# Performance work log

Hardware: AMD Instinct MI355X
Metric: run time of the kernel (lower is better)

## Reference

```python
import jax, jax.numpy as jnp
import numpy as np

B, N, E0, F_IN, H, EMB, VEC, DPI = 1024, 256, 2048, 6, 32, 32, 26, 512


def setup_inputs() -> dict:
    key = jax.random.key(0)
    ks = jax.random.split(key, 16)
    # fixed urban scene graph, shared by every batch element, with self-loops
    src0 = jax.random.randint(ks[0], (E0,), 0, N, dtype=jnp.int32)
    dst0 = jax.random.randint(ks[1], (E0,), 0, N, dtype=jnp.int32)
    loops = jnp.arange(N, dtype=jnp.int32)
    src = jnp.concatenate([src0, loops])
    dst = jnp.concatenate([dst0, loops])

    s = 0.05
    return {
        "graph_feats": jax.random.normal(ks[2], (B, N, F_IN), jnp.float32),
        "vector": jax.random.normal(ks[3], (B, VEC), jnp.float32),
        "src": src,
        "dst": dst,
        "W1": jax.random.normal(ks[4], (F_IN, H), jnp.float32) * s,
        "b1": jnp.zeros((H,), jnp.float32),
        "W2": jax.random.normal(ks[5], (H, H), jnp.float32) * s,
        "b2": jnp.zeros((H,), jnp.float32),
        "W3": jax.random.normal(ks[6], (H, H), jnp.float32) * s,
        "b3": jnp.zeros((H,), jnp.float32),
        "W_emb": jax.random.normal(ks[7], (H, EMB), jnp.float32) * s,
        "b_emb": jnp.zeros((EMB,), jnp.float32),
        "W_pi": jax.random.normal(ks[8], (VEC + EMB, DPI), jnp.float32) * s,
        "b_pi": jnp.zeros((DPI,), jnp.float32),
        "W_vf": jax.random.normal(ks[9], (VEC + EMB, DPI), jnp.float32) * s,
        "b_vf": jnp.zeros((DPI,), jnp.float32),
    }


def _edge_norm(src, dst, n_nodes):
    # DGL GraphConv norm='both': out_deg(src)^-1/2 * in_deg(dst)^-1/2
    ones = jnp.ones(src.shape[0], jnp.float32)
    deg_out = jax.ops.segment_sum(ones, src, num_segments=n_nodes)
    deg_in = jax.ops.segment_sum(ones, dst, num_segments=n_nodes)
    inv_o = jnp.where(deg_out > 0, deg_out ** -0.5, 0.0)
    inv_i = jnp.where(deg_in > 0, deg_in ** -0.5, 0.0)
    return inv_o[src] * inv_i[dst]  # [E]


def _gconv(h, src, dst, norm, W, b):
    # h: [B, N, F]; symmetric-normalized aggregation then linear (DGL GraphConv)
    msg = h[:, src, :] * norm[None, :, None]          # [B, E, F]
    agg = jnp.zeros_like(h).at[:, dst, :].add(msg)     # [B, N, F]
    return agg @ W + b


def reference(graph_feats, vector, src, dst, W1, b1, W2, b2, W3, b3,
              W_emb, b_emb, W_pi, b_pi, W_vf, b_vf):
    n_nodes = graph_feats.shape[1]
    norm = _edge_norm(src, dst, n_nodes)
    h = jax.nn.relu(_gconv(graph_feats, src, dst, norm, W1, b1))
    h = jax.nn.relu(_gconv(h, src, dst, norm, W2, b2))
    h = jax.nn.relu(_gconv(h, src, dst, norm, W3, b3))  # three_layers=True
    hg = jnp.mean(h, axis=1)                 # dgl.mean_nodes -> [B, H]
    emb = hg @ W_emb + b_emb                 # [B, EMB]
    comb = jnp.concatenate([vector[:, :26], emb], axis=1)  # [B, 58]
    pi = jax.nn.relu(comb @ W_pi + b_pi)
    vf = jax.nn.relu(comb @ W_vf + b_vf)
    return pi, vf
```

## Files before the change

### kernel.cpp

```cpp
#include <hip/hip_runtime.h>
#include <hip/hip_fp16.h>

#define B_    1024
#define N_    256
#define E_    2304
#define EPT_  9
#define FIN_  6
#define VEC_  26
#define HSTR_ 40

typedef _Float16 half8 __attribute__((ext_vector_type(8)));
typedef float    f32x4 __attribute__((ext_vector_type(4)));

__global__ __launch_bounds__(256) void fused_kernel(
    const float* __restrict__ gf,
    const float* __restrict__ vec,
    const int* __restrict__ src, const int* __restrict__ dst,
    const float* __restrict__ W1, const float* __restrict__ b1,
    const float* __restrict__ W2, const float* __restrict__ b2,
    const float* __restrict__ W3, const float* __restrict__ b3,
    const float* __restrict__ We, const float* __restrict__ be,
    const float* __restrict__ Wpi, const float* __restrict__ bpi,
    const float* __restrict__ Wvf, const float* __restrict__ bvf,
    float2* __restrict__ out)
{
    __shared__ __align__(16) __half hbuf[N_ * HSTR_];
    __shared__ unsigned int packedE[E_];
    __shared__ float part[8 * 33];
    __shared__ float hgl[32];
    __shared__ float comb[VEC_ + 32];
    __shared__ int   wsum[4];

    const int t = threadIdx.x;
    const int b = blockIdx.x;
    const int lane = t & 63, wv = t >> 6;

    int*   deg_o  = (int*)hbuf;
    int*   deg_i  = (int*)hbuf + 256;
    int*   scanA  = (int*)hbuf + 512;
    int*   cursor = (int*)hbuf + 768;
    int*   perm   = (int*)hbuf + 1024;
    float* inv_o  = (float*)hbuf + 1280;
    float* inv_i  = (float*)hbuf + 1536;
    int*   bcnt   = (int*)hbuf + 1792;
    int*   boff   = (int*)hbuf + 1856;

    deg_o[t] = 0; deg_i[t] = 0;
    if (t < 64) bcnt[t] = 0;
    __syncthreads();

    int sB[EPT_], dB[EPT_];
#pragma unroll
    for (int i = 0; i < EPT_; ++i) { int e = t + 256 * i; sB[i] = src[e]; dB[i] = dst[e]; }
#pragma unroll
    for (int i = 0; i < EPT_; ++i) { atomicAdd(&deg_o[sB[i]], 1); atomicAdd(&deg_i[dB[i]], 1); }
    __syncthreads();

    const int dI = deg_i[t];
    {
        int dO = deg_o[t];
        inv_o[t] = dO > 0 ? rsqrtf((float)dO) : 0.f;
        inv_i[t] = dI > 0 ? rsqrtf((float)dI) : 0.f;
    }
    int x = dI;
#pragma unroll
    for (int d = 1; d < 64; d <<= 1) {
        int y = __shfl_up(x, d, 64);
        if (lane >= d) x += y;
    }
    if (lane == 63) wsum[wv] = x;
    const int bucket = dI > 63 ? 63 : dI;
    atomicAdd(&bcnt[bucket], 1);
    __syncthreads();

    {
        int prefix = 0;
#pragma unroll
        for (int w = 0; w < 3; ++w) if (w < wv) prefix += wsum[w];
        int incl = x + prefix;
        scanA[t]  = incl;
        cursor[t] = incl - dI;
    }
    if (t < 64) {
        int c = bcnt[t], xx = c;
#pragma unroll
        for (int d = 1; d < 64; d <<= 1) {
            int y = __shfl_up(xx, d, 64);
            if (lane >= d) xx += y;
        }
        boff[t] = xx - c;
    }
    __syncthreads();

    { int pos = atomicAdd(&boff[bucket], 1); perm[pos] = t; }
#pragma unroll
    for (int i = 0; i < EPT_; ++i) {
        int s = sB[i], dd = dB[i];
        int pos = atomicAdd(&cursor[dd], 1);
        float nrm = inv_o[s] * inv_i[dd];
        unsigned short h = __half_as_ushort(__float2half(nrm));
        packedE[pos] = ((unsigned int)s << 16) | (unsigned int)h;
    }
    __syncthreads();

    const int node = perm[t];
    const int end  = scanA[node];
    const int beg  = end - deg_i[node];
    __syncthreads();

    {
        const float* g = gf + (size_t)b * (N_ * FIN_);
        for (int i = t; i < N_ * 8; i += 256) {
            int n = i >> 3, k = i & 7;
            hbuf[n * HSTR_ + k] = __float2half((k < FIN_) ? g[n * FIN_ + k] : 0.f);
        }
    }
    __syncthreads();

    const __half2 z2 = __float2half2_rn(0.f);

    {
        __half2 a2[4] = {z2, z2, z2, z2};
        for (int e = beg; e < end; ++e) {
            unsigned int u = packedE[e];
            __half2 w2 = __half2half2(__ushort_as_half((unsigned short)(u & 0xffffu)));
            union { float4 f4; __half2 h2[4]; } r;
            r.f4 = *(const float4*)&hbuf[(u >> 16) * HSTR_];
#pragma unroll
            for (int q = 0; q < 4; ++q) a2[q] = __hfma2(w2, r.h2[q], a2[q]);
        }
        float a[FIN_], o[32];
#pragma unroll
        for (int k = 0; k < FIN_; ++k)
            a[k] = (k & 1) ? __high2float(a2[k >> 1]) : __low2float(a2[k >> 1]);
#pragma unroll
        for (int j = 0; j < 32; ++j) o[j] = b1[j];
#pragma unroll
        for (int k = 0; k < FIN_; ++k) {
            float ak = a[k];
            const float* wr = &W1[k * 32];
#pragma unroll
            for (int j = 0; j < 32; ++j) o[j] += ak * wr[j];
        }
        __syncthreads();
        union { float4 f4; __half2 h2[4]; } w;
        float4* row = (float4*)&hbuf[node * HSTR_];
#pragma unroll
        for (int q = 0; q < 4; ++q) {
#pragma unroll
            for (int r = 0; r < 4; ++r)
                w.h2[r] = __floats2half2_rn(fmaxf(o[8*q + 2*r], 0.f), fmaxf(o[8*q + 2*r + 1], 0.f));
            row[q] = w.f4;
        }
    }
    __syncthreads();

    const int m16  = lane & 15;
    const int q4   = lane >> 4;
    const int slab = wv * 64;

    for (int L = 0; L < 2; ++L) {
        const float* Wl = (L == 0) ? W2 : W3;
        const float* Bl = (L == 0) ? b2 : b3;

        half8 bfrag[2];
        float bias_c[2];
#pragma unroll
        for (int h = 0; h < 2; ++h) {
            int col = m16 + 16 * h;
#pragma unroll
            for (int j = 0; j < 8; ++j)
                bfrag[h][j] = (_Float16)Wl[(q4 * 8 + j) * 32 + col];
            bias_c[h] = Bl[col];
        }

        __half2 acc2[16];
#pragma unroll
        for (int j = 0; j < 16; ++j) acc2[j] = z2;
        for (int e = beg; e < end; ++e) {
            unsigned int u = packedE[e];
            __half2 w2 = __half2half2(__ushort_as_half((unsigned short)(u & 0xffffu)));
            const float4* hr = (const float4*)&hbuf[(u >> 16) * HSTR_];
            union { float4 f4; __half2 h2[4]; } r0, r1, r2, r3;
            r0.f4 = hr[0]; r1.f4 = hr[1]; r2.f4 = hr[2]; r3.f4 = hr[3];
#pragma unroll
            for (int q = 0; q < 4; ++q) {
                acc2[q]      = __hfma2(w2, r0.h2[q], acc2[q]);
                acc2[4 + q]  = __hfma2(w2, r1.h2[q], acc2[4 + q]);
                acc2[8 + q]  = __hfma2(w2, r2.h2[q], acc2[8 + q]);
                acc2[12 + q] = __hfma2(w2, r3.h2[q], acc2[12 + q]);
            }
        }
        __syncthreads();
        {
            union { float4 f4; __half2 h2[4]; } w;
            float4* row = (float4*)&hbuf[node * HSTR_];
#pragma unroll
            for (int q = 0; q < 4; ++q) {
#pragma unroll
                for (int r = 0; r < 4; ++r) w.h2[r] = acc2[4 * q + r];
                row[q] = w.f4;
            }
        }
        __syncthreads();

        half8 afrag[4];
#pragma unroll
        for (int g = 0; g < 4; ++g) {
            union { float4 f4; half8 h8; } u;
            u.f4 = *(const float4*)&hbuf[(slab + g * 16 + m16) * HSTR_ + q4 * 8];
            afrag[g] = u.h8;
        }
        f32x4 D[4][2];
#pragma unroll
        for (int g = 0; g < 4; ++g) {
#pragma unroll
            for (int h = 0; h < 2; ++h) {
                f32x4 c = {bias_c[h], bias_c[h], bias_c[h], bias_c[h]};
                D[g][h] = __builtin_amdgcn_mfma_f32_16x16x32_f16(afrag[g], bfrag[h], c, 0, 0, 0);
            }
        }
#pragma unroll
        for (int g = 0; g < 4; ++g) {
#pragma unroll
            for (int h = 0; h < 2; ++h) {
#pragma unroll
                for (int r = 0; r < 4; ++r) {
                    float v = fmaxf(D[g][h][r], 0.f);
                    hbuf[(slab + g * 16 + q4 * 4 + r) * HSTR_ + h * 16 + m16] = __float2half(v);
                }
            }
        }
        __syncthreads();
    }

    {
        int j = t & 31, g8 = t >> 5;
        float s = 0.f;
        for (int i = 0; i < 32; ++i)
            s += __half2float(hbuf[(g8 * 32 + i) * HSTR_ + j]);
        part[g8 * 33 + j] = s;
    }
    __syncthreads();
    if (t < 32) {
        float sum = 0.f;
#pragma unroll
        for (int g8 = 0; g8 < 8; ++g8) sum += part[g8 * 33 + t];
        hgl[t] = sum * (1.0f / 256.0f);
    }
    __syncthreads();

    if (t < 32) {
        float v = be[t];
#pragma unroll
        for (int j = 0; j < 32; ++j) v += hgl[j] * We[j * 32 + t];
        comb[VEC_ + t] = v;
    }
    if (t < VEC_) comb[t] = vec[b * VEC_ + t];
    __syncthreads();

    {
        float p0 = bpi[2 * t], p1 = bpi[2 * t + 1];
        float v0 = bvf[2 * t], v1 = bvf[2 * t + 1];
        const float2* Wp = (const float2*)Wpi;
        const float2* Wv = (const float2*)Wvf;
        for (int k = 0; k < VEC_ + 32; ++k) {
            float c = comb[k];
            float2 a = Wp[k * 256 + t];
            p0 += c * a.x; p1 += c * a.y;
            float2 d = Wv[k * 256 + t];
            v0 += c * d.x; v1 += c * d.y;
        }
        out[b * 256 + t]          = make_float2(fmaxf(p0, 0.f), fmaxf(p1, 0.f));
        out[262144 + b * 256 + t] = make_float2(fmaxf(v0, 0.f), fmaxf(v1, 0.f));
    }
}

extern "C" void kernel_launch(void* const* d_in, const int* in_sizes, int n_in,
                              void* d_out, int out_size, void* d_ws, size_t ws_size,
                              hipStream_t stream)
{
    fused_kernel<<<B_, 256, 0, stream>>>(
        (const float*)d_in[0], (const float*)d_in[1],
        (const int*)d_in[2], (const int*)d_in[3],
        (const float*)d_in[4], (const float*)d_in[5],
        (const float*)d_in[6], (const float*)d_in[7],
        (const float*)d_in[8], (const float*)d_in[9],
        (const float*)d_in[10], (const float*)d_in[11],
        (const float*)d_in[12], (const float*)d_in[13],
        (const float*)d_in[14], (const float*)d_in[15],
        (float2*)d_out);
}
```

Measured before the change: 119.0 us.

## Process two batch elements per block to amortize graph preprocessing

Each block now runs 512 threads and handles two batch elements. The degree counting, normalization, CSR sort and edge packing are done once by the first 256 threads and shared by both halves, which have separate hbuf slabs. In the final MLP each half computes one head (pi or vf) for both batch elements, so every weight load is reused across two samples. The cost is more shared memory per block (two 20KB hbufs) and idle threads during preprocessing, which may lower occupancy.

```diff
diff --git a/kernel.cpp b/kernel.cpp
--- a/kernel.cpp
+++ b/kernel.cpp
@@ -8,11 +8,12 @@
 #define FIN_  6
 #define VEC_  26
 #define HSTR_ 40
+#define BPB_  2
 
 typedef _Float16 half8 __attribute__((ext_vector_type(8)));
 typedef float    f32x4 __attribute__((ext_vector_type(4)));
 
-__global__ __launch_bounds__(256) void fused_kernel(
+__global__ __launch_bounds__(512) void fused_kernel(
     const float* __restrict__ gf,
     const float* __restrict__ vec,
     const int* __restrict__ src, const int* __restrict__ dst,
@@ -24,56 +25,65 @@
     const float* __restrict__ Wvf, const float* __restrict__ bvf,
     float2* __restrict__ out)
 {
-    __shared__ __align__(16) __half hbuf[N_ * HSTR_];
+    __shared__ __align__(16) __half hbuf[BPB_][N_ * HSTR_];
     __shared__ unsigned int packedE[E_];
-    __shared__ float part[8 * 33];
-    __shared__ float hgl[32];
-    __shared__ float comb[VEC_ + 32];
+    __shared__ float part[BPB_][8 * 33];
+    __shared__ float hgl[BPB_][32];
+    __shared__ float combS[BPB_][64];
     __shared__ int   wsum[4];
 
-    const int t = threadIdx.x;
-    const int b = blockIdx.x;
+    const int t  = threadIdx.x;
+    const int u  = t & 255;
+    const int bh = t >> 8;
+    const int b0 = blockIdx.x * BPB_;
     const int lane = t & 63, wv = t >> 6;
 
-    int*   deg_o  = (int*)hbuf;
-    int*   deg_i  = (int*)hbuf + 256;
-    int*   scanA  = (int*)hbuf + 512;
-    int*   cursor = (int*)hbuf + 768;
-    int*   perm   = (int*)hbuf + 1024;
-    float* inv_o  = (float*)hbuf + 1280;
-    float* inv_i  = (float*)hbuf + 1536;
-    int*   bcnt   = (int*)hbuf + 1792;
-    int*   boff   = (int*)hbuf + 1856;
-
-    deg_o[t] = 0; deg_i[t] = 0;
-    if (t < 64) bcnt[t] = 0;
+    int*   deg_o  = (int*)&hbuf[0][0];
+    int*   deg_i  = (int*)&hbuf[0][0] + 256;
+    int*   scanA  = (int*)&hbuf[0][0] + 512;
+    int*   cursor = (int*)&hbuf[0][0] + 768;
+    int*   perm   = (int*)&hbuf[0][0] + 1024;
+    float* inv_o  = (float*)&hbuf[0][0] + 1280;
+    float* inv_i  = (float*)&hbuf[0][0] + 1536;
+    int*   bcnt   = (int*)&hbuf[0][0] + 1792;
+    int*   boff   = (int*)&hbuf[0][0] + 1856;
+
+    if (t < 256) {
+        deg_o[t] = 0; deg_i[t] = 0;
+        if (t < 64) bcnt[t] = 0;
+    }
     __syncthreads();
 
     int sB[EPT_], dB[EPT_];
-#pragma unroll
-    for (int i = 0; i < EPT_; ++i) { int e = t + 256 * i; sB[i] = src[e]; dB[i] = dst[e]; }
-#pragma unroll
-    for (int i = 0; i < EPT_; ++i) { atomicAdd(&deg_o[sB[i]], 1); atomicAdd(&deg_i[dB[i]], 1); }
-    __syncthreads();
-
-    const int dI = deg_i[t];
-    {
-        int dO = deg_o[t];
-        inv_o[t] = dO > 0 ? rsqrtf((float)dO) : 0.f;
-        inv_i[t] = dI > 0 ? rsqrtf((float)dI) : 0.f;
-    }
-    int x = dI;
-#pragma unroll
-    for (int d = 1; d < 64; d <<= 1) {
-        int y = __shfl_up(x, d, 64);
-        if (lane >= d) x += y;
-    }
-    if (lane == 63) wsum[wv] = x;
-    const int bucket = dI > 63 ? 63 : dI;
-    atomicAdd(&bcnt[bucket], 1);
-    __syncthreads();
-
-    {
+    if (t < 256) {
+#pragma unroll
+        for (int i = 0; i < EPT_; ++i) { int e = t + 256 * i; sB[i] = src[e]; dB[i] = dst[e]; }
+#pragma unroll
+        for (int i = 0; i < EPT_; ++i) { atomicAdd(&deg_o[sB[i]], 1); atomicAdd(&deg_i[dB[i]], 1); }
+    }
+    __syncthreads();
+
+    int x = 0, dI = 0, bucket = 0;
+    if (t < 256) {
+        dI = deg_i[t];
+        {
+            int dO = deg_o[t];
+            inv_o[t] = dO > 0 ? rsqrtf((float)dO) : 0.f;
+            inv_i[t] = dI > 0 ? rsqrtf((float)dI) : 0.f;
+        }
+        x = dI;
+#pragma unroll
+        for (int d = 1; d < 64; d <<= 1) {
+            int y = __shfl_up(x, d, 64);
+            if (lane >= d) x += y;
+        }
+        if (lane == 63) wsum[wv] = x;
+        bucket = dI > 63 ? 63 : dI;
+        atomicAdd(&bcnt[bucket], 1);
+    }
+    __syncthreads();
+
+    if (t < 256) {
         int prefix = 0;
 #pragma unroll
         for (int w = 0; w < 3; ++w) if (w < wv) prefix += wsum[w];
@@ -92,27 +102,29 @@
     }
     __syncthreads();
 
-    { int pos = atomicAdd(&boff[bucket], 1); perm[pos] = t; }
-#pragma unroll
-    for (int i = 0; i < EPT_; ++i) {
-        int s = sB[i], dd = dB[i];
-        int pos = atomicAdd(&cursor[dd], 1);
-        float nrm = inv_o[s] * inv_i[dd];
-        unsigned short h = __half_as_ushort(__float2half(nrm));
-        packedE[pos] = ((unsigned int)s << 16) | (unsigned int)h;
-    }
-    __syncthreads();
-
-    const int node = perm[t];
+    if (t < 256) {
+        { int pos = atomicAdd(&boff[bucket], 1); perm[pos] = t; }
+#pragma unroll
+        for (int i = 0; i < EPT_; ++i) {
+            int s = sB[i], dd = dB[i];
+            int pos = atomicAdd(&cursor[dd], 1);
+            float nrm = inv_o[s] * inv_i[dd];
+            unsigned short hh = __half_as_ushort(__float2half(nrm));
+            packedE[pos] = ((unsigned int)s << 16) | (unsigned int)hh;
+        }
+    }
+    __syncthreads();
+
+    const int node = perm[u];
     const int end  = scanA[node];
     const int beg  = end - deg_i[node];
     __syncthreads();
 
     {
-        const float* g = gf + (size_t)b * (N_ * FIN_);
-        for (int i = t; i < N_ * 8; i += 256) {
+        const float* g = gf + (size_t)(b0 + bh) * (N_ * FIN_);
+        for (int i = u; i < N_ * 8; i += 256) {
             int n = i >> 3, k = i & 7;
-            hbuf[n * HSTR_ + k] = __float2half((k < FIN_) ? g[n * FIN_ + k] : 0.f);
+            hbuf[bh][n * HSTR_ + k] = __float2half((k < FIN_) ? g[n * FIN_ + k] : 0.f);
         }
     }
     __syncthreads();
@@ -122,29 +134,27 @@
     {
         __half2 a2[4] = {z2, z2, z2, z2};
         for (int e = beg; e < end; ++e) {
-            unsigned int u = packedE[e];
-            __half2 w2 = __half2half2(__ushort_as_half((unsigned short)(u & 0xffffu)));
+            unsigned int uu = packedE[e];
+            __half2 w2 = __half2half2(__ushort_as_half((unsigned short)(uu & 0xffffu)));
+            int ro = (uu >> 16) * HSTR_;
             union { float4 f4; __half2 h2[4]; } r;
-            r.f4 = *(const float4*)&hbuf[(u >> 16) * HSTR_];
+            r.f4 = *(const float4*)&hbuf[bh][ro];
 #pragma unroll
             for (int q = 0; q < 4; ++q) a2[q] = __hfma2(w2, r.h2[q], a2[q]);
         }
-        float a[FIN_], o[32];
-#pragma unroll
-        for (int k = 0; k < FIN_; ++k)
-            a[k] = (k & 1) ? __high2float(a2[k >> 1]) : __low2float(a2[k >> 1]);
+        float o[32];
 #pragma unroll
         for (int j = 0; j < 32; ++j) o[j] = b1[j];
 #pragma unroll
         for (int k = 0; k < FIN_; ++k) {
-            float ak = a[k];
+            float ak = (k & 1) ? __high2float(a2[k >> 1]) : __low2float(a2[k >> 1]);
             const float* wr = &W1[k * 32];
 #pragma unroll
             for (int j = 0; j < 32; ++j) o[j] += ak * wr[j];
         }
         __syncthreads();
         union { float4 f4; __half2 h2[4]; } w;
-        float4* row = (float4*)&hbuf[node * HSTR_];
+        float4* row = (float4*)&hbuf[bh][node * HSTR_];
 #pragma unroll
         for (int q = 0; q < 4; ++q) {
 #pragma unroll
@@ -157,7 +167,8 @@
 
     const int m16  = lane & 15;
     const int q4   = lane >> 4;
-    const int slab = wv * 64;
+    const int slab = (wv & 3) * 64;
+    const int wb   = wv >> 2;
 
     for (int L = 0; L < 2; ++L) {
         const float* Wl = (L == 0) ? W2 : W3;
@@ -166,21 +177,22 @@
         half8 bfrag[2];
         float bias_c[2];
 #pragma unroll
-        for (int h = 0; h < 2; ++h) {
-            int col = m16 + 16 * h;
+        for (int cb = 0; cb < 2; ++cb) {
+            int col = m16 + 16 * cb;
 #pragma unroll
             for (int j = 0; j < 8; ++j)
-                bfrag[h][j] = (_Float16)Wl[(q4 * 8 + j) * 32 + col];
-            bias_c[h] = Bl[col];
+                bfrag[cb][j] = (_Float16)Wl[(q4 * 8 + j) * 32 + col];
+            bias_c[cb] = Bl[col];
         }
 
         __half2 acc2[16];
 #pragma unroll
         for (int j = 0; j < 16; ++j) acc2[j] = z2;
         for (int e = beg; e < end; ++e) {
-            unsigned int u = packedE[e];
-            __half2 w2 = __half2half2(__ushort_as_half((unsigned short)(u & 0xffffu)));
-            const float4* hr = (const float4*)&hbuf[(u >> 16) * HSTR_];
+            unsigned int uu = packedE[e];
+            __half2 w2 = __half2half2(__ushort_as_half((unsigned short)(uu & 0xffffu)));
+            int ro = (uu >> 16) * HSTR_;
+            const float4* hr = (const float4*)&hbuf[bh][ro];
             union { float4 f4; __half2 h2[4]; } r0, r1, r2, r3;
             r0.f4 = hr[0]; r1.f4 = hr[1]; r2.f4 = hr[2]; r3.f4 = hr[3];
 #pragma unroll
@@ -194,7 +206,7 @@
         __syncthreads();
         {
             union { float4 f4; __half2 h2[4]; } w;
-            float4* row = (float4*)&hbuf[node * HSTR_];
+            float4* row = (float4*)&hbuf[bh][node * HSTR_];
 #pragma unroll
             for (int q = 0; q < 4; ++q) {
 #pragma unroll
@@ -204,75 +216,84 @@
         }
         __syncthreads();
 
-        half8 afrag[4];
-#pragma unroll
-        for (int g = 0; g < 4; ++g) {
-            union { float4 f4; half8 h8; } u;
-            u.f4 = *(const float4*)&hbuf[(slab + g * 16 + m16) * HSTR_ + q4 * 8];
-            afrag[g] = u.h8;
-        }
-        f32x4 D[4][2];
-#pragma unroll
-        for (int g = 0; g < 4; ++g) {
-#pragma unroll
-            for (int h = 0; h < 2; ++h) {
-                f32x4 c = {bias_c[h], bias_c[h], bias_c[h], bias_c[h]};
-                D[g][h] = __builtin_amdgcn_mfma_f32_16x16x32_f16(afrag[g], bfrag[h], c, 0, 0, 0);
-            }
-        }
-#pragma unroll
-        for (int g = 0; g < 4; ++g) {
-#pragma unroll
-            for (int h = 0; h < 2; ++h) {
-#pragma unroll
-                for (int r = 0; r < 4; ++r) {
-                    float v = fmaxf(D[g][h][r], 0.f);
-                    hbuf[(slab + g * 16 + q4 * 4 + r) * HSTR_ + h * 16 + m16] = __float2half(v);
+        {
+            half8 afrag[4];
+#pragma unroll
+            for (int g = 0; g < 4; ++g) {
+                union { float4 f4; half8 h8; } uf;
+                uf.f4 = *(const float4*)&hbuf[wb][(slab + g * 16 + m16) * HSTR_ + q4 * 8];
+                afrag[g] = uf.h8;
+            }
+            f32x4 D[4][2];
+#pragma unroll
+            for (int g = 0; g < 4; ++g) {
+#pragma unroll
+                for (int cb = 0; cb < 2; ++cb) {
+                    f32x4 c = {bias_c[cb], bias_c[cb], bias_c[cb], bias_c[cb]};
+                    D[g][cb] = __builtin_amdgcn_mfma_f32_16x16x32_f16(afrag[g], bfrag[cb], c, 0, 0, 0);
                 }
             }
+#pragma unroll
+            for (int g = 0; g < 4; ++g) {
+#pragma unroll
+                for (int cb = 0; cb < 2; ++cb) {
+#pragma unroll
+                    for (int r = 0; r < 4; ++r) {
+                        float v = fmaxf(D[g][cb][r], 0.f);
+                        hbuf[wb][(slab + g * 16 + q4 * 4 + r) * HSTR_ + cb * 16 + m16] = __float2half(v);
+                    }
+                }
+            }
         }
         __syncthreads();
     }
 
     {
-        int j = t & 31, g8 = t >> 5;
+        int j = u & 31, g8 = u >> 5;
         float s = 0.f;
         for (int i = 0; i < 32; ++i)
-            s += __half2float(hbuf[(g8 * 32 + i) * HSTR_ + j]);
-        part[g8 * 33 + j] = s;
-    }
-    __syncthreads();
-    if (t < 32) {
+            s += __half2float(hbuf[bh][(g8 * 32 + i) * HSTR_ + j]);
+        part[bh][g8 * 33 + j] = s;
+    }
+    __syncthreads();
+    if (t < 64) {
+        int bb = t >> 5, j = t & 31;
         float sum = 0.f;
 #pragma unroll
-        for (int g8 = 0; g8 < 8; ++g8) sum += part[g8 * 33 + t];
-        hgl[t] = sum * (1.0f / 256.0f);
-    }
-    __syncthreads();
-
-    if (t < 32) {
-        float v = be[t];
-#pragma unroll
-        for (int j = 0; j < 32; ++j) v += hgl[j] * We[j * 32 + t];
-        comb[VEC_ + t] = v;
-    }
-    if (t < VEC_) comb[t] = vec[b * VEC_ + t];
+        for (int g8 = 0; g8 < 8; ++g8) sum += part[bb][g8 * 33 + j];
+        hgl[bb][j] = sum * (1.0f / 256.0f);
+    }
+    if (t < BPB_ * VEC_) {
+        int bb = t / VEC_, j = t - bb * VEC_;
+        combS[bb][j] = vec[(b0 + bb) * VEC_ + j];
+    }
+    __syncthreads();
+
+    if (t < 64) {
+        int bb = t >> 5, j = t & 31;
+        float v = be[j];
+#pragma unroll
+        for (int k = 0; k < 32; ++k) v += hgl[bb][k] * We[k * 32 + j];
+        combS[bb][VEC_ + j] = v;
+    }
     __syncthreads();
 
     {
-        float p0 = bpi[2 * t], p1 = bpi[2 * t + 1];
-        float v0 = bvf[2 * t], v1 = bvf[2 * t + 1];
-        const float2* Wp = (const float2*)Wpi;
-        const float2* Wv = (const float2*)Wvf;
+        const float* Wm = (bh == 0) ? Wpi : Wvf;
+        const float* bm = (bh == 0) ? bpi : bvf;
+        const float2 bp = ((const float2*)bm)[u];
+        float2 a0 = bp, a1 = bp;
+        const float2* Wr = (const float2*)Wm;
         for (int k = 0; k < VEC_ + 32; ++k) {
-            float c = comb[k];
-            float2 a = Wp[k * 256 + t];
-            p0 += c * a.x; p1 += c * a.y;
-            float2 d = Wv[k * 256 + t];
-            v0 += c * d.x; v1 += c * d.y;
-        }
-        out[b * 256 + t]          = make_float2(fmaxf(p0, 0.f), fmaxf(p1, 0.f));
-        out[262144 + b * 256 + t] = make_float2(fmaxf(v0, 0.f), fmaxf(v1, 0.f));
+            float2 a = Wr[k * 256 + u];
+            float c0 = combS[0][k];
+            float c1 = combS[1][k];
+            a0.x += c0 * a.x; a0.y += c0 * a.y;
+            a1.x += c1 * a.x; a1.y += c1 * a.y;
+        }
+        int base = bh * 262144;
+        out[base + b0 * 256 + u]       = make_float2(fmaxf(a0.x, 0.f), fmaxf(a0.y, 0.f));
+        out[base + (b0 + 1) * 256 + u] = make_float2(fmaxf(a1.x, 0.f), fmaxf(a1.y, 0.f));
     }
 }
 
@@ -280,7 +301,7 @@
                               void* d_out, int out_size, void* d_ws, size_t ws_size,
                               hipStream_t stream)
 {
-    fused_kernel<<<B_, 256, 0, stream>>>(
+    fused_kernel<<<B_ / BPB_, 512, 0, stream>>>(
         (const float*)d_in[0], (const float*)d_in[1],
         (const int*)d_in[2], (const int*)d_in[3],
         (const float*)d_in[4], (const float*)d_in[5],
```

After: 114.0 us (median of 2 runs). 1.04x faster.
